# Optimization experiments

Hardware: AMD Instinct MI355X
Metric: run time of the kernel (lower is better)

Reference implementation:

```python
import jax, jax.numpy as jnp
import numpy as np

B, S, H, NH = 8, 1024, 1024, 16
D = H // NH          # attention_hidden_size = 64
V = S                # v_size must equal seq_len (mask broadcast)


def setup_inputs() -> dict:
    key = jax.random.key(0)
    ks = jax.random.split(key, 9)
    s = 0.02
    return {
        "q": jax.random.normal(ks[0], (B, S, H), jnp.float32),
        "k": jax.random.normal(ks[1], (B, S, H), jnp.float32),
        "v": jax.random.normal(ks[2], (B, S, H), jnp.float32),
        # per-head Q/K projections, stacked over heads: (NH, H, D)
        "Wq": jax.random.normal(ks[3], (NH, H, D), jnp.float32) * s,
        "bq": jax.random.normal(ks[4], (NH, D), jnp.float32) * s,
        "Wk": jax.random.normal(ks[5], (NH, H, D), jnp.float32) * s,
        "bk": jax.random.normal(ks[6], (NH, D), jnp.float32) * s,
        # shared V projection hidden -> v_size
        "Wv": jax.random.normal(ks[7], (H, V), jnp.float32) * s,
        "bv": jax.random.normal(ks[8], (V,), jnp.float32) * s,
    }


def reference(q, k, v, Wq, bq, Wk, bk, Wv, bv):
    d = Wq.shape[-1]
    scale = d ** (-0.5)
    # per-head projections, heads vectorized into leading axis n
    qh = jnp.einsum('bsh,nhd->nbsd', q, Wq) + bq[:, None, None, :]
    kh = jnp.einsum('bth,nhd->nbtd', k, Wk) + bk[:, None, None, :]
    vv = jnp.einsum('bth,hv->btv', v, Wv) + bv          # shared V: (B,S,V)
    seq = q.shape[1]
    mask = jnp.triu(jnp.full((seq, seq), -jnp.inf, dtype=q.dtype), 1)
    scores = jnp.einsum('nbsd,nbtd->nbst', qh, kh) * scale + mask
    p = jax.nn.softmax(scores, axis=-1)                  # (NH,B,S,S)
    # matmul against shared V then mean over heads (== stack + mean)
    out = jnp.einsum('nbst,btv->nbsv', p, vv).mean(axis=0)
    return out
```

## Files before the change

kernel.cpp:

```cpp
#include <hip/hip_runtime.h>


#define NHEAD 16
#define BATCH 8
#define SEQ   1024
#define HID   1024
#define DHEAD 64

typedef _Float16 f16;
typedef _Float16 f16x4 __attribute__((ext_vector_type(4)));
typedef _Float16 f16x8 __attribute__((ext_vector_type(8)));
typedef float    f32x4 __attribute__((ext_vector_type(4)));

__device__ __forceinline__ f32x4 mfma16(f16x8 a, f16x8 b, f32x4 c) {
  return __builtin_amdgcn_mfma_f32_16x16x32_f16(a, b, c, 0, 0, 0);
}

__device__ __forceinline__ void gload16(const f16* g, f16* l) {
  __builtin_amdgcn_global_load_lds(
      (const __attribute__((address_space(1))) void*)g,
      (__attribute__((address_space(3))) void*)l, 16, 0, 0);
}

__device__ __forceinline__ void stage_swz(const f16* __restrict__ g, int ldg,
                                          f16* lds, int nch, int tid) {
  for (int idx = tid; idx < nch; idx += 256) {
    int row = idx >> 3, c16 = idx & 7;
    int sc = c16 ^ (row & 7);
    gload16(g + (size_t)row * ldg + sc * 8, lds + (size_t)(idx & ~63) * 8);
  }
}

__device__ __forceinline__ f16x8 lds_frag(const f16* lds, int row, int c16) {
  int sc = c16 ^ (row & 7);
  return *(const f16x8*)&lds[row * 64 + sc * 8];
}


__global__ __launch_bounds__(256) void conv3(
    const float* __restrict__ q, const float* __restrict__ k,
    const float* __restrict__ v, f16* __restrict__ dq, f16* __restrict__ dk,
    f16* __restrict__ dv) {
  const float* src = blockIdx.z == 0 ? q : blockIdx.z == 1 ? k : v;
  f16* dst = blockIdx.z == 0 ? dq : blockIdx.z == 1 ? dk : dv;
  int i = (blockIdx.x * 256 + threadIdx.x) * 4;
  float4 f = *(const float4*)(src + i);
  f16x4 o = { (f16)f.x, (f16)f.y, (f16)f.z, (f16)f.w };
  *(f16x4*)(dst + i) = o;
}

__global__ __launch_bounds__(256) void tconv2(
    const float* __restrict__ s0, const float* __restrict__ s1,
    f16* __restrict__ d0, f16* __restrict__ d1, int R, int C, int half) {
  int z = blockIdx.z;
  const float* src; f16* dst;
  if (z < half) { src = s0 + (size_t)z * R * C; dst = d0 + (size_t)z * R * C; }
  else { src = s1 + (size_t)(z - half) * R * C; dst = d1 + (size_t)(z - half) * R * C; }
  const int c0 = blockIdx.x * 64, r0 = blockIdx.y * 64;
  __shared__ f16 t[64][72];
  const int tid = threadIdx.x;
#pragma unroll
  for (int i = 0; i < 4; i++) {
    int chunk = tid + i * 256;
    int row = chunk >> 4, c4 = chunk & 15;
    float4 f = *(const float4*)&src[(size_t)(r0 + row) * C + c0 + c4 * 4];
    f16x4 h = { (f16)f.x, (f16)f.y, (f16)f.z, (f16)f.w };
    *(f16x4*)&t[row][c4 * 4] = h;
  }
  __syncthreads();
  const int cc = tid >> 2, q = tid & 3;
  f16 tmp[16];
#pragma unroll
  for (int j = 0; j < 16; j++) tmp[j] = t[q * 16 + j][cc];
  *(f16x8*)&dst[(size_t)(c0 + cc) * R + r0 + q * 16] = *(f16x8*)&tmp[0];
  *(f16x8*)&dst[(size_t)(c0 + cc) * R + r0 + q * 16 + 8] = *(f16x8*)&tmp[8];
}


__device__ __forceinline__ void gemm_core(
    const f16* __restrict__ A, const f16* __restrict__ Bt, int K, int Kend,
    int row0, int col0, f16* la, f16* lb, int tid, f32x4 (&acc)[4][4]) {
  const int lane = tid & 63;
  const int wr = (tid >> 6) >> 1, wc = (tid >> 6) & 1;
  for (int k0 = 0; k0 < Kend; k0 += 64) {
    __syncthreads();
    stage_swz(A + (size_t)row0 * K + k0, K, la, 1024, tid);
    stage_swz(Bt + (size_t)col0 * K + k0, K, lb, 1024, tid);
    __syncthreads();
#pragma unroll
    for (int ks = 0; ks < 2; ks++) {
      f16x8 af[4], bfr[4];
#pragma unroll
      for (int mi = 0; mi < 4; mi++)
        af[mi] = lds_frag(la, wr * 64 + mi * 16 + (lane & 15), ks * 4 + (lane >> 4));
#pragma unroll
      for (int ni = 0; ni < 4; ni++)
        bfr[ni] = lds_frag(lb, wc * 64 + ni * 16 + (lane & 15), ks * 4 + (lane >> 4));
#pragma unroll
      for (int mi = 0; mi < 4; mi++)
#pragma unroll
        for (int ni = 0; ni < 4; ni++)
          acc[mi][ni] = mfma16(af[mi], bfr[ni], acc[mi][ni]);
    }
  }
}


__global__ __launch_bounds__(256) void proj_gemm(
    const f16* __restrict__ A0, const f16* __restrict__ A1,
    const f16* __restrict__ Bt0, const f16* __restrict__ Bt1,
    const float* __restrict__ bias0, const float* __restrict__ bias1,
    f16* __restrict__ C0, f16* __restrict__ C1) {
  const int which = blockIdx.z;
  const f16* A = which ? A1 : A0;
  const f16* Bt = which ? Bt1 : Bt0;
  const float* bias = which ? bias1 : bias0;
  f16* C = which ? C1 : C0;
  __shared__ alignas(16) f16 la[128 * 64];
  __shared__ alignas(16) f16 lb[128 * 64];
  const int tid = threadIdx.x, lane = tid & 63;
  const int wr = (tid >> 6) >> 1, wc = (tid >> 6) & 1;
  const int row0 = blockIdx.x * 128, col0 = blockIdx.y * 128;
  f32x4 acc[4][4];
#pragma unroll
  for (int i = 0; i < 4; i++)
#pragma unroll
    for (int j = 0; j < 4; j++) acc[i][j] = (f32x4){0.f, 0.f, 0.f, 0.f};
  gemm_core(A, Bt, HID, HID, row0, col0, la, lb, tid, acc);
#pragma unroll
  for (int mi = 0; mi < 4; mi++)
#pragma unroll
    for (int ni = 0; ni < 4; ni++)
#pragma unroll
      for (int r = 0; r < 4; r++) {
        int m = row0 + wr * 64 + mi * 16 + ((lane >> 4) << 2) + r;
        int j = col0 + wc * 64 + ni * 16 + (lane & 15);
        float val = acc[mi][ni][r] + bias[j];
        int bb = m >> 10, s = m & 1023, hn = j >> 6, d = j & 63;
        C[(((size_t)hn * BATCH + bb) * SEQ + s) * DHEAD + d] = (f16)val;
      }
}


__global__ __launch_bounds__(256) void vv_gemm(
    const f16* __restrict__ A, const f16* __restrict__ Bt,
    const float* __restrict__ bias, f16* __restrict__ C) {
  __shared__ alignas(16) f16 la[128 * 64];
  __shared__ alignas(16) f16 lb[128 * 64];
  const int tid = threadIdx.x, lane = tid & 63;
  const int wr = (tid >> 6) >> 1, wc = (tid >> 6) & 1;
  const int row0 = blockIdx.x * 128, col0 = blockIdx.y * 128;
  f32x4 acc[4][4];
#pragma unroll
  for (int i = 0; i < 4; i++)
#pragma unroll
    for (int j = 0; j < 4; j++) acc[i][j] = (f32x4){0.f, 0.f, 0.f, 0.f};
  gemm_core(A, Bt, HID, HID, row0, col0, la, lb, tid, acc);
#pragma unroll
  for (int mi = 0; mi < 4; mi++)
#pragma unroll
    for (int ni = 0; ni < 4; ni++)
#pragma unroll
      for (int r = 0; r < 4; r++) {
        int m = row0 + wr * 64 + mi * 16 + ((lane >> 4) << 2) + r;
        int j = col0 + wc * 64 + ni * 16 + (lane & 15);
        float val = acc[mi][ni][r] + bias[m];
        int bb = j >> 10, t = j & 1023;
        C[((size_t)bb * SEQ + m) * SEQ + t] = (f16)val;
      }
}


__global__ __launch_bounds__(256) void attn_stats(
    const f16* __restrict__ QH, const f16* __restrict__ KH,
    float* __restrict__ madj_ws) {
  const int flat = blockIdx.x;
  const int sb = 15 - (flat >> 7);
  const int nb = flat & 127;
  const int n = nb >> 3, b = nb & 7;
  const int s0 = sb * 64;
  const f16* qh = QH + ((size_t)n * BATCH + b) * SEQ * DHEAD;
  const f16* kh = KH + ((size_t)n * BATCH + b) * SEQ * DHEAD;

  const int tid = threadIdx.x, lane = tid & 63, wave = tid >> 6;
  const int lr = lane & 15;
  const int qg = lane >> 4;
  const int ch = qg << 3;

  f16x8 aq[4][2];
#pragma unroll
  for (int fi = 0; fi < 4; fi++) {
    const f16* qp = qh + (size_t)(s0 + fi * 16 + lr) * 64 + ch;
    aq[fi][0] = *(const f16x8*)qp;
    aq[fi][1] = *(const f16x8*)(qp + 32);
  }

  const float sl2e = 0.125f * 1.44269504088896f;
  float l_p[16];
#pragma unroll
  for (int i = 0; i < 16; i++) l_p[i] = 0.f;

  const int nt = (sb + 1) * 4;
  const int dstart = sb * 4;
  const int njw = (nt - wave + 3) >> 2;
  const f16* kp = kh + (size_t)lr * 64 + ch;

  f16x8 kA0, kA1, kB0, kB1;

#define LDK(jj, X0, X1) { const f16* p_ = kp + (size_t)(jj) * 1024; \
    X0 = *(const f16x8*)p_; X1 = *(const f16x8*)(p_ + 32); }

#define COMP(jj, X0, X1) { \
    f32x4 c_[4]; \
    _Pragma("unroll") for (int fi = 0; fi < 4; fi++) { \
      f32x4 cc = (f32x4){0.f, 0.f, 0.f, 0.f}; \
      cc = mfma16(aq[fi][0], X0, cc); cc = mfma16(aq[fi][1], X1, cc); \
      c_[fi] = cc; } \
    if ((jj) < dstart) { \
      _Pragma("unroll") for (int fi = 0; fi < 4; fi++) \
        _Pragma("unroll") for (int r = 0; r < 4; r++) \
          l_p[fi * 4 + r] += exp2f(c_[fi][r] * sl2e); \
    } else { \
      int tg_ = (jj) * 16 + lr; \
      _Pragma("unroll") for (int fi = 0; fi < 4; fi++) \
        _Pragma("unroll") for (int r = 0; r < 4; r++) { \
          int sg_ = s0 + fi * 16 + qg * 4 + r; \
          l_p[fi * 4 + r] += (tg_ <= sg_) ? exp2f(c_[fi][r] * sl2e) : 0.f; } } }

  LDK(wave, kA0, kA1);
  int idx = 0;
  for (; idx + 2 <= njw; idx += 2) {
    LDK(wave + (idx + 1) * 4, kB0, kB1);
    COMP(wave + idx * 4, kA0, kA1);
    if (idx + 2 < njw) LDK(wave + (idx + 2) * 4, kA0, kA1);
    COMP(wave + (idx + 1) * 4, kB0, kB1);
  }
  if (idx < njw) COMP(wave + idx * 4, kA0, kA1);
#undef LDK
#undef COMP

  __shared__ float lds_l[4][64];
#pragma unroll
  for (int i = 0; i < 16; i++) {
    float l = l_p[i];
    l += __shfl_xor(l, 1); l += __shfl_xor(l, 2);
    l += __shfl_xor(l, 4); l += __shfl_xor(l, 8);
    if (lr == 0) lds_l[wave][(i >> 2) * 16 + qg * 4 + (i & 3)] = l;
  }
  __syncthreads();
  if (tid < 64) {
    float l = lds_l[0][tid] + lds_l[1][tid] + lds_l[2][tid] + lds_l[3][tid];
    madj_ws[((size_t)n * BATCH + b) * SEQ + s0 + tid] = -__log2f(l) - 4.0f;
  }
}


__global__ __launch_bounds__(256) void attn_pbar(
    const f16* __restrict__ QH, const f16* __restrict__ KH,
    const float* __restrict__ madj_ws, f16* __restrict__ pp) {
  const int flat = blockIdx.x;
  const int wg = (flat & 7) * 144 + (flat >> 3);
  int f = wg % 72, sb = 0, tcid = 0;
  const int y = wg / 72;
  for (int s = 15; s >= 0; --s) {
    int c = (s >> 1) + 1;
    if (f < c) { sb = s; tcid = f; break; }
    f -= c;
  }
  const int s0 = sb * 64, t0 = tcid * 128;
  const int b = y >> 1, gg = y & 1;
  const int n0 = gg * 8;

  const int tid = threadIdx.x, lane = tid & 63, wave = tid >> 6;
  const float sl2e = 0.125f * 1.44269504088896f;
  const int lr = lane & 15, qg = lane >> 4, ch = qg << 3;

  int ntc = ((s0 + 63 - t0) >> 4) + 1;
  ntc = ntc > 8 ? 8 : ntc;
  const int j0 = wave, j1 = wave + 4;
  const bool has1 = j1 < ntc;

  const size_t HS = (size_t)BATCH * SEQ * DHEAD;
  const size_t MHS = (size_t)BATCH * SEQ;
  const f16* qbase = QH + (size_t)b * SEQ * DHEAD;
  const f16* kbase = KH + (size_t)b * SEQ * DHEAD;
  const float* mabase = madj_ws + (size_t)b * SEQ;

  float paccA[16], paccB[16];
#pragma unroll
  for (int i = 0; i < 16; i++) { paccA[i] = 0.f; paccB[i] = 0.f; }

  for (int nn = 0; nn < 8; nn++) {
    const int n = n0 + nn;
    const f16* qh = qbase + (size_t)n * HS;
    const f16* kh = kbase + (size_t)n * HS;

    f16x8 kA0, kA1, kB0, kB1;
    {
      const f16* p = kh + (size_t)(t0 + j0 * 16 + lr) * 64 + ch;
      kA0 = *(const f16x8*)p; kA1 = *(const f16x8*)(p + 32);
    }
    if (has1) {
      const f16* p = kh + (size_t)(t0 + j1 * 16 + lr) * 64 + ch;
      kB0 = *(const f16x8*)p; kB1 = *(const f16x8*)(p + 32);
    }
    f16x8 aq[4][2];
#pragma unroll
    for (int fi = 0; fi < 4; fi++) {
      const f16* qp = qh + (size_t)(s0 + fi * 16 + lr) * 64 + ch;
      aq[fi][0] = *(const f16x8*)qp;
      aq[fi][1] = *(const f16x8*)(qp + 32);
    }
    float ma[4][4];
#pragma unroll
    for (int fi = 0; fi < 4; fi++) {
      float4 m4 = *(const float4*)&mabase[(size_t)n * MHS + s0 + fi * 16 + qg * 4];
      ma[fi][0] = m4.x; ma[fi][1] = m4.y; ma[fi][2] = m4.z; ma[fi][3] = m4.w;
    }

#define PCOMP(jj, X0, X1, PC) { \
    int tg_ = t0 + (jj) * 16 + lr; \
    _Pragma("unroll") for (int fi = 0; fi < 4; fi++) { \
      f32x4 cc = (f32x4){0.f, 0.f, 0.f, 0.f}; \
      cc = mfma16(aq[fi][0], X0, cc); cc = mfma16(aq[fi][1], X1, cc); \
      _Pragma("unroll") for (int r = 0; r < 4; r++) { \
        int sg_ = s0 + fi * 16 + qg * 4 + r; \
        float p_ = exp2f(fmaf(cc[r], sl2e, ma[fi][r])); \
        PC[fi * 4 + r] += (tg_ <= sg_) ? p_ : 0.f; } } }

    PCOMP(j0, kA0, kA1, paccA);
    if (has1) PCOMP(j1, kB0, kB1, paccB);
#undef PCOMP
  }

  f16* out = pp + ((size_t)gg * BATCH + b) * SEQ * SEQ;
#pragma unroll
  for (int fi = 0; fi < 4; fi++) {
#pragma unroll
    for (int r = 0; r < 4; r++) {
      size_t row = (size_t)(s0 + fi * 16 + qg * 4 + r) * SEQ;
      out[row + t0 + j0 * 16 + lr] = (f16)paccA[fi * 4 + r];
      out[row + t0 + j1 * 16 + lr] = (f16)paccB[fi * 4 + r];
    }
  }
}


__global__ __launch_bounds__(256) void pv_gemm(
    const f16* __restrict__ pp, const f16* __restrict__ vvT,
    float* __restrict__ out) {
  const int b = blockIdx.z;
  const size_t GS = (size_t)BATCH * SEQ * SEQ;
  const f16* A0 = pp + (size_t)b * SEQ * SEQ;
  const f16* A1 = pp + GS + (size_t)b * SEQ * SEQ;
  const f16* Bt = vvT + (size_t)b * SEQ * SEQ;
  __shared__ alignas(16) f16 la0[128 * 64];
  __shared__ alignas(16) f16 la1[128 * 64];
  __shared__ alignas(16) f16 lb[128 * 64];
  const int tid = threadIdx.x, lane = tid & 63;
  const int wr = (tid >> 6) >> 1, wc = (tid >> 6) & 1;
  const int row0 = blockIdx.x * 128, col0 = blockIdx.y * 128;
  const int Kend = (row0 + 128 < SEQ) ? row0 + 128 : SEQ;

  f32x4 acc[4][4];
#pragma unroll
  for (int i = 0; i < 4; i++)
#pragma unroll
    for (int j = 0; j < 4; j++) acc[i][j] = (f32x4){0.f, 0.f, 0.f, 0.f};

  for (int k0 = 0; k0 < Kend; k0 += 64) {
    __syncthreads();
    stage_swz(A0 + (size_t)row0 * SEQ + k0, SEQ, la0, 1024, tid);
    stage_swz(A1 + (size_t)row0 * SEQ + k0, SEQ, la1, 1024, tid);
    stage_swz(Bt + (size_t)col0 * SEQ + k0, SEQ, lb, 1024, tid);
    __syncthreads();
#pragma unroll
    for (int ks = 0; ks < 2; ks++) {
      f16x8 a0[4], a1[4], bfr[4];
#pragma unroll
      for (int mi = 0; mi < 4; mi++) {
        a0[mi] = lds_frag(la0, wr * 64 + mi * 16 + (lane & 15), ks * 4 + (lane >> 4));
        a1[mi] = lds_frag(la1, wr * 64 + mi * 16 + (lane & 15), ks * 4 + (lane >> 4));
      }
#pragma unroll
      for (int ni = 0; ni < 4; ni++)
        bfr[ni] = lds_frag(lb, wc * 64 + ni * 16 + (lane & 15), ks * 4 + (lane >> 4));
#pragma unroll
      for (int mi = 0; mi < 4; mi++)
#pragma unroll
        for (int ni = 0; ni < 4; ni++) {
          acc[mi][ni] = mfma16(a0[mi], bfr[ni], acc[mi][ni]);
          acc[mi][ni] = mfma16(a1[mi], bfr[ni], acc[mi][ni]);
        }
    }
  }

#pragma unroll
  for (int mi = 0; mi < 4; mi++)
#pragma unroll
    for (int ni = 0; ni < 4; ni++)
#pragma unroll
      for (int r = 0; r < 4; r++) {
        int m = row0 + wr * 64 + mi * 16 + ((lane >> 4) << 2) + r;
        int j = col0 + wc * 64 + ni * 16 + (lane & 15);
        out[(size_t)b * SEQ * SEQ + (size_t)m * SEQ + j] = acc[mi][ni][r];
      }
}


extern "C" void kernel_launch(void* const* d_in, const int* in_sizes, int n_in,
                              void* d_out, int out_size, void* d_ws, size_t ws_size,
                              hipStream_t stream) {
  (void)in_sizes; (void)n_in; (void)out_size; (void)ws_size;
  const float* q  = (const float*)d_in[0];
  const float* k  = (const float*)d_in[1];
  const float* v  = (const float*)d_in[2];
  const float* Wq = (const float*)d_in[3];
  const float* bq = (const float*)d_in[4];
  const float* Wk = (const float*)d_in[5];
  const float* bk = (const float*)d_in[6];
  const float* Wv = (const float*)d_in[7];
  const float* bv = (const float*)d_in[8];
  float* out = (float*)d_out;

  const size_t EL  = (size_t)BATCH * SEQ * HID;
  const size_t WEL = (size_t)NHEAD * HID * DHEAD;

  char* ws = (char*)d_ws;
  f16* qbf = (f16*)ws;  ws += EL * 2;
  f16* kbf = (f16*)ws;  ws += EL * 2;
  f16* vbf = (f16*)ws;  ws += EL * 2;
  f16* WqT = (f16*)ws;  ws += WEL * 2;
  f16* WkT = (f16*)ws;  ws += WEL * 2;
  f16* WvT = (f16*)ws;  ws += WEL * 2;
  f16* QHb = (f16*)ws;  ws += EL * 2;
  f16* KHb = (f16*)ws;  ws += EL * 2;
  f16* vvT = (f16*)ws;  ws += EL * 2;
  float* madj_ws = (float*)ws; ws += (size_t)NHEAD * BATCH * SEQ * 4;
  f16* pp = qbf;

  conv3<<<dim3(8192, 1, 3), 256, 0, stream>>>(q, k, v, qbf, kbf, vbf);
  tconv2<<<dim3(1, 16, 32), 256, 0, stream>>>(Wq, Wk, WqT, WkT, 1024, 64, 16);
  tconv2<<<dim3(16, 16, 1), 256, 0, stream>>>(Wv, Wv, WvT, WvT, 1024, 1024, 1);

  proj_gemm<<<dim3(64, 8, 2), 256, 0, stream>>>(qbf, kbf, WqT, WkT, bq, bk,
                                                QHb, KHb);
  vv_gemm<<<dim3(8, 64, 1), 256, 0, stream>>>(WvT, vbf, bv, vvT);

  attn_stats<<<dim3(2048, 1, 1), 256, 0, stream>>>(QHb, KHb, madj_ws);
  attn_pbar<<<dim3(1152, 1, 1), 256, 0, stream>>>(QHb, KHb, madj_ws, pp);
  pv_gemm<<<dim3(8, 8, 8), 256, 0, stream>>>(pp, vvT, out);
}
```

Baseline: 240.7 us.

## Halve attn_pbar row tile, double-buffer per-head loads, skip mask on interior tiles

attn_pbar now covers 32 query rows per workgroup instead of 64, which doubles the grid to 2304 blocks and halves the per-thread accumulators. Launch bounds ask for 4 waves per SIMD. Q, K and row-max loads for the next head are software-pipelined into a second register set so they overlap the MFMA and exp work of the current head. The causal-mask compare is skipped on tiles that lie fully below the diagonal. The cost is more redundant K loads across the extra blocks and higher register pressure from the double buffers.

```diff
diff --git a/kernel.cpp b/kernel.cpp
--- a/kernel.cpp
+++ b/kernel.cpp
@@ -255,19 +255,20 @@
 }
 
 
-__global__ __launch_bounds__(256) void attn_pbar(
+__global__ __launch_bounds__(256, 4) void attn_pbar(
     const f16* __restrict__ QH, const f16* __restrict__ KH,
     const float* __restrict__ madj_ws, f16* __restrict__ pp) {
   const int flat = blockIdx.x;
-  const int wg = (flat & 7) * 144 + (flat >> 3);
-  int f = wg % 72, sb = 0, tcid = 0;
-  const int y = wg / 72;
-  for (int s = 15; s >= 0; --s) {
-    int c = (s >> 1) + 1;
+  const int wg = (flat & 7) * 288 + (flat >> 3);
+  int f = wg % 144;
+  const int y = wg / 144;
+  int sb = 0, tcid = 0;
+  for (int s = 31; s >= 0; --s) {
+    int c = (s >> 2) + 1;
     if (f < c) { sb = s; tcid = f; break; }
     f -= c;
   }
-  const int s0 = sb * 64, t0 = tcid * 128;
+  const int s0 = sb * 32, t0 = tcid * 128;
   const int b = y >> 1, gg = y & 1;
   const int n0 = gg * 8;
 
@@ -275,67 +276,77 @@
   const float sl2e = 0.125f * 1.44269504088896f;
   const int lr = lane & 15, qg = lane >> 4, ch = qg << 3;
 
-  int ntc = ((s0 + 63 - t0) >> 4) + 1;
+  int ntc = ((s0 + 31 - t0) >> 4) + 1;
   ntc = ntc > 8 ? 8 : ntc;
   const int j0 = wave, j1 = wave + 4;
-  const bool has1 = j1 < ntc;
+  const bool c0 = j0 < ntc, c1 = j1 < ntc;
 
   const size_t HS = (size_t)BATCH * SEQ * DHEAD;
   const size_t MHS = (size_t)BATCH * SEQ;
-  const f16* qbase = QH + (size_t)b * SEQ * DHEAD;
-  const f16* kbase = KH + (size_t)b * SEQ * DHEAD;
-  const float* mabase = madj_ws + (size_t)b * SEQ;
-
-  float paccA[16], paccB[16];
-#pragma unroll
-  for (int i = 0; i < 16; i++) { paccA[i] = 0.f; paccB[i] = 0.f; }
-
-  for (int nn = 0; nn < 8; nn++) {
-    const int n = n0 + nn;
-    const f16* qh = qbase + (size_t)n * HS;
-    const f16* kh = kbase + (size_t)n * HS;
-
-    f16x8 kA0, kA1, kB0, kB1;
-    {
-      const f16* p = kh + (size_t)(t0 + j0 * 16 + lr) * 64 + ch;
-      kA0 = *(const f16x8*)p; kA1 = *(const f16x8*)(p + 32);
-    }
-    if (has1) {
-      const f16* p = kh + (size_t)(t0 + j1 * 16 + lr) * 64 + ch;
-      kB0 = *(const f16x8*)p; kB1 = *(const f16x8*)(p + 32);
-    }
-    f16x8 aq[4][2];
-#pragma unroll
-    for (int fi = 0; fi < 4; fi++) {
-      const f16* qp = qh + (size_t)(s0 + fi * 16 + lr) * 64 + ch;
-      aq[fi][0] = *(const f16x8*)qp;
-      aq[fi][1] = *(const f16x8*)(qp + 32);
-    }
-    float ma[4][4];
-#pragma unroll
-    for (int fi = 0; fi < 4; fi++) {
-      float4 m4 = *(const float4*)&mabase[(size_t)n * MHS + s0 + fi * 16 + qg * 4];
-      ma[fi][0] = m4.x; ma[fi][1] = m4.y; ma[fi][2] = m4.z; ma[fi][3] = m4.w;
-    }
-
-#define PCOMP(jj, X0, X1, PC) { \
+  const f16* qptr = QH + ((size_t)n0 * BATCH + b) * SEQ * DHEAD +
+                    (size_t)(s0 + lr) * 64 + ch;
+  const f16* kptr = KH + ((size_t)n0 * BATCH + b) * SEQ * DHEAD +
+                    (size_t)(t0 + j0 * 16 + lr) * 64 + ch;
+  const float* mptr = madj_ws + ((size_t)n0 * BATCH + b) * SEQ + s0 + qg * 4;
+
+  float paccA[8], paccB[8];
+#pragma unroll
+  for (int i = 0; i < 8; i++) { paccA[i] = 0.f; paccB[i] = 0.f; }
+
+  f16x8 Xq0a, Xq0b, Xq1a, Xq1b, Xk0a, Xk0b, Xk1a, Xk1b;
+  float4 Xm0, Xm1;
+  f16x8 Yq0a, Yq0b, Yq1a, Yq1b, Yk0a, Yk0b, Yk1a, Yk1b;
+  float4 Ym0, Ym1;
+
+#define LOADH(h, q0a, q0b, q1a, q1b, k0a, k0b, k1a, k1b, m0, m1) { \
+    const f16* qp_ = qptr + (size_t)(h) * HS; \
+    q0a = *(const f16x8*)qp_;          q0b = *(const f16x8*)(qp_ + 32); \
+    q1a = *(const f16x8*)(qp_ + 1024); q1b = *(const f16x8*)(qp_ + 1024 + 32); \
+    const f16* kp_ = kptr + (size_t)(h) * HS; \
+    k0a = *(const f16x8*)kp_;          k0b = *(const f16x8*)(kp_ + 32); \
+    k1a = *(const f16x8*)(kp_ + 4096); k1b = *(const f16x8*)(kp_ + 4096 + 32); \
+    const float* mp_ = mptr + (size_t)(h) * MHS; \
+    m0 = *(const float4*)mp_; m1 = *(const float4*)(mp_ + 16); }
+
+#define TILE(jj, ka, kb, qa, qb, mm, pc, fi) { \
+    f32x4 cc = (f32x4){0.f, 0.f, 0.f, 0.f}; \
+    cc = mfma16(qa, ka, cc); \
+    cc = mfma16(qb, kb, cc); \
     int tg_ = t0 + (jj) * 16 + lr; \
-    _Pragma("unroll") for (int fi = 0; fi < 4; fi++) { \
-      f32x4 cc = (f32x4){0.f, 0.f, 0.f, 0.f}; \
-      cc = mfma16(aq[fi][0], X0, cc); cc = mfma16(aq[fi][1], X1, cc); \
-      _Pragma("unroll") for (int r = 0; r < 4; r++) { \
-        int sg_ = s0 + fi * 16 + qg * 4 + r; \
-        float p_ = exp2f(fmaf(cc[r], sl2e, ma[fi][r])); \
-        PC[fi * 4 + r] += (tg_ <= sg_) ? p_ : 0.f; } } }
-
-    PCOMP(j0, kA0, kA1, paccA);
-    if (has1) PCOMP(j1, kB0, kB1, paccB);
-#undef PCOMP
-  }
+    bool msk_ = (t0 + (jj) * 16 + 15) > (s0 + (fi) * 16); \
+    _Pragma("unroll") for (int r = 0; r < 4; r++) { \
+      float p_ = exp2f(fmaf(cc[r], sl2e, mm[r])); \
+      if (msk_) p_ = (tg_ <= s0 + (fi) * 16 + qg * 4 + r) ? p_ : 0.f; \
+      pc[(fi) * 4 + r] += p_; } }
+
+#define COMPH(q0a, q0b, q1a, q1b, k0a, k0b, k1a, k1b, m0, m1) { \
+    float mm0_[4] = {m0.x, m0.y, m0.z, m0.w}; \
+    float mm1_[4] = {m1.x, m1.y, m1.z, m1.w}; \
+    if (c0) { \
+      TILE(j0, k0a, k0b, q0a, q0b, mm0_, paccA, 0); \
+      TILE(j0, k0a, k0b, q1a, q1b, mm1_, paccA, 1); \
+    } \
+    if (c1) { \
+      TILE(j1, k1a, k1b, q0a, q0b, mm0_, paccB, 0); \
+      TILE(j1, k1a, k1b, q1a, q1b, mm1_, paccB, 1); \
+    } }
+
+  LOADH(0, Xq0a, Xq0b, Xq1a, Xq1b, Xk0a, Xk0b, Xk1a, Xk1b, Xm0, Xm1);
+#pragma unroll
+  for (int h = 0; h < 8; h += 2) {
+    LOADH(h + 1, Yq0a, Yq0b, Yq1a, Yq1b, Yk0a, Yk0b, Yk1a, Yk1b, Ym0, Ym1);
+    COMPH(Xq0a, Xq0b, Xq1a, Xq1b, Xk0a, Xk0b, Xk1a, Xk1b, Xm0, Xm1);
+    if (h + 2 < 8)
+      LOADH(h + 2, Xq0a, Xq0b, Xq1a, Xq1b, Xk0a, Xk0b, Xk1a, Xk1b, Xm0, Xm1);
+    COMPH(Yq0a, Yq0b, Yq1a, Yq1b, Yk0a, Yk0b, Yk1a, Yk1b, Ym0, Ym1);
+  }
+#undef LOADH
+#undef TILE
+#undef COMPH
 
   f16* out = pp + ((size_t)gg * BATCH + b) * SEQ * SEQ;
 #pragma unroll
-  for (int fi = 0; fi < 4; fi++) {
+  for (int fi = 0; fi < 2; fi++) {
 #pragma unroll
     for (int r = 0; r < 4; r++) {
       size_t row = (size_t)(s0 + fi * 16 + qg * 4 + r) * SEQ;
@@ -448,6 +459,6 @@
   vv_gemm<<<dim3(8, 64, 1), 256, 0, stream>>>(WvT, vbf, bv, vvT);
 
   attn_stats<<<dim3(2048, 1, 1), 256, 0, stream>>>(QHb, KHb, madj_ws);
-  attn_pbar<<<dim3(1152, 1, 1), 256, 0, stream>>>(QHb, KHb, madj_ws, pp);
+  attn_pbar<<<dim3(2304, 1, 1), 256, 0, stream>>>(QHb, KHb, madj_ws, pp);
   pv_gemm<<<dim3(8, 8, 8), 256, 0, stream>>>(pp, vvT, out);
 }
```

Result: slower. 247.0 us (+2.6%).

## Rewrite P-bar kernel as LDS-staged 128x128 tiled GEMM over lower triangle

Applied to the files above, without the earlier changes.

Replaces the per-wave register-fragment attn_pbar kernel (64x128 tiles, direct global loads of Q/K per head) with a 128x128 tiled kernel that stages Q and K head tiles into swizzled LDS and computes a 4x4 MFMA block per wave. Only lower-triangular tile pairs are launched, and the causal mask is applied only on diagonal tiles. This is meant to raise data reuse and MFMA density and cut redundant global loads. In exchange it uses fewer, larger blocks (576 vs 1152), adds two syncthreads per head, and does more masked work inside the diagonal tiles.

```diff
diff --git a/kernel.cpp b/kernel.cpp
--- a/kernel.cpp
+++ b/kernel.cpp
@@ -255,94 +255,103 @@
 }
 
 
-__global__ __launch_bounds__(256) void attn_pbar(
+__global__ __launch_bounds__(256) void pbar_gemm(
     const f16* __restrict__ QH, const f16* __restrict__ KH,
     const float* __restrict__ madj_ws, f16* __restrict__ pp) {
-  const int flat = blockIdx.x;
-  const int wg = (flat & 7) * 144 + (flat >> 3);
-  int f = wg % 72, sb = 0, tcid = 0;
-  const int y = wg / 72;
-  for (int s = 15; s >= 0; --s) {
-    int c = (s >> 1) + 1;
-    if (f < c) { sb = s; tcid = f; break; }
-    f -= c;
-  }
-  const int s0 = sb * 64, t0 = tcid * 128;
-  const int b = y >> 1, gg = y & 1;
-  const int n0 = gg * 8;
-
-  const int tid = threadIdx.x, lane = tid & 63, wave = tid >> 6;
+  int ti = blockIdx.x, rb = 0, cb = 0;
+  {
+    int t = ti;
+#pragma unroll
+    for (int r = 0; r < 8; ++r) {
+      if (t <= r) { rb = r; cb = t; break; }
+      t -= r + 1;
+    }
+  }
+  const int r0 = rb * 128, c0 = cb * 128;
+  const int y = blockIdx.y;
+  const int b = y >> 1, g = y & 1;
+  const int n0 = g * 8;
+  const bool diag = (rb == cb);
+
+  __shared__ alignas(16) f16 la[128 * 64];
+  __shared__ alignas(16) f16 lb[128 * 64];
+
+  const int tid = threadIdx.x, lane = tid & 63;
+  const int wr = (tid >> 6) >> 1, wc = (tid >> 6) & 1;
+  const int lr = lane & 15, qg = lane >> 4;
   const float sl2e = 0.125f * 1.44269504088896f;
-  const int lr = lane & 15, qg = lane >> 4, ch = qg << 3;
-
-  int ntc = ((s0 + 63 - t0) >> 4) + 1;
-  ntc = ntc > 8 ? 8 : ntc;
-  const int j0 = wave, j1 = wave + 4;
-  const bool has1 = j1 < ntc;
-
-  const size_t HS = (size_t)BATCH * SEQ * DHEAD;
-  const size_t MHS = (size_t)BATCH * SEQ;
-  const f16* qbase = QH + (size_t)b * SEQ * DHEAD;
-  const f16* kbase = KH + (size_t)b * SEQ * DHEAD;
-  const float* mabase = madj_ws + (size_t)b * SEQ;
-
-  float paccA[16], paccB[16];
-#pragma unroll
-  for (int i = 0; i < 16; i++) { paccA[i] = 0.f; paccB[i] = 0.f; }
-
-  for (int nn = 0; nn < 8; nn++) {
-    const int n = n0 + nn;
-    const f16* qh = qbase + (size_t)n * HS;
-    const f16* kh = kbase + (size_t)n * HS;
-
-    f16x8 kA0, kA1, kB0, kB1;
-    {
-      const f16* p = kh + (size_t)(t0 + j0 * 16 + lr) * 64 + ch;
-      kA0 = *(const f16x8*)p; kA1 = *(const f16x8*)(p + 32);
+
+  f32x4 pacc[4][4];
+#pragma unroll
+  for (int i = 0; i < 4; i++)
+#pragma unroll
+    for (int j = 0; j < 4; j++) pacc[i][j] = (f32x4){0.f, 0.f, 0.f, 0.f};
+
+  for (int h = 0; h < 8; ++h) {
+    const int n = n0 + h;
+    const f16* qh = QH + ((size_t)n * BATCH + b) * SEQ * DHEAD;
+    const f16* kh = KH + ((size_t)n * BATCH + b) * SEQ * DHEAD;
+
+    __syncthreads();
+    stage_swz(qh + (size_t)r0 * 64, 64, la, 1024, tid);
+    stage_swz(kh + (size_t)c0 * 64, 64, lb, 1024, tid);
+    __syncthreads();
+
+    f32x4 acc[4][4];
+#pragma unroll
+    for (int i = 0; i < 4; i++)
+#pragma unroll
+      for (int j = 0; j < 4; j++) acc[i][j] = (f32x4){0.f, 0.f, 0.f, 0.f};
+
+#pragma unroll
+    for (int ks = 0; ks < 2; ks++) {
+      f16x8 af[4], bfr[4];
+#pragma unroll
+      for (int mi = 0; mi < 4; mi++)
+        af[mi] = lds_frag(la, wr * 64 + mi * 16 + lr, ks * 4 + qg);
+#pragma unroll
+      for (int ni = 0; ni < 4; ni++)
+        bfr[ni] = lds_frag(lb, wc * 64 + ni * 16 + lr, ks * 4 + qg);
+#pragma unroll
+      for (int mi = 0; mi < 4; mi++)
+#pragma unroll
+        for (int ni = 0; ni < 4; ni++)
+          acc[mi][ni] = mfma16(af[mi], bfr[ni], acc[mi][ni]);
     }
-    if (has1) {
-      const f16* p = kh + (size_t)(t0 + j1 * 16 + lr) * 64 + ch;
-      kB0 = *(const f16x8*)p; kB1 = *(const f16x8*)(p + 32);
+
+    const float* mb = madj_ws + ((size_t)n * BATCH + b) * SEQ + r0 +
+                      wr * 64 + qg * 4;
+#pragma unroll
+    for (int mi = 0; mi < 4; mi++) {
+      float4 m4 = *(const float4*)(mb + mi * 16);
+      float ma[4] = {m4.x, m4.y, m4.z, m4.w};
+#pragma unroll
+      for (int ni = 0; ni < 4; ni++) {
+        int tg = c0 + wc * 64 + ni * 16 + lr;
+#pragma unroll
+        for (int r = 0; r < 4; r++) {
+          float p = exp2f(fmaf(acc[mi][ni][r], sl2e, ma[r]));
+          if (diag) {
+            int sg = r0 + wr * 64 + mi * 16 + qg * 4 + r;
+            p = (tg <= sg) ? p : 0.f;
+          }
+          pacc[mi][ni][r] += p;
+        }
+      }
     }
-    f16x8 aq[4][2];
-#pragma unroll
-    for (int fi = 0; fi < 4; fi++) {
-      const f16* qp = qh + (size_t)(s0 + fi * 16 + lr) * 64 + ch;
-      aq[fi][0] = *(const f16x8*)qp;
-      aq[fi][1] = *(const f16x8*)(qp + 32);
-    }
-    float ma[4][4];
-#pragma unroll
-    for (int fi = 0; fi < 4; fi++) {
-      float4 m4 = *(const float4*)&mabase[(size_t)n * MHS + s0 + fi * 16 + qg * 4];
-      ma[fi][0] = m4.x; ma[fi][1] = m4.y; ma[fi][2] = m4.z; ma[fi][3] = m4.w;
-    }
-
-#define PCOMP(jj, X0, X1, PC) { \
-    int tg_ = t0 + (jj) * 16 + lr; \
-    _Pragma("unroll") for (int fi = 0; fi < 4; fi++) { \
-      f32x4 cc = (f32x4){0.f, 0.f, 0.f, 0.f}; \
-      cc = mfma16(aq[fi][0], X0, cc); cc = mfma16(aq[fi][1], X1, cc); \
-      _Pragma("unroll") for (int r = 0; r < 4; r++) { \
-        int sg_ = s0 + fi * 16 + qg * 4 + r; \
-        float p_ = exp2f(fmaf(cc[r], sl2e, ma[fi][r])); \
-        PC[fi * 4 + r] += (tg_ <= sg_) ? p_ : 0.f; } } }
-
-    PCOMP(j0, kA0, kA1, paccA);
-    if (has1) PCOMP(j1, kB0, kB1, paccB);
-#undef PCOMP
-  }
-
-  f16* out = pp + ((size_t)gg * BATCH + b) * SEQ * SEQ;
-#pragma unroll
-  for (int fi = 0; fi < 4; fi++) {
-#pragma unroll
-    for (int r = 0; r < 4; r++) {
-      size_t row = (size_t)(s0 + fi * 16 + qg * 4 + r) * SEQ;
-      out[row + t0 + j0 * 16 + lr] = (f16)paccA[fi * 4 + r];
-      out[row + t0 + j1 * 16 + lr] = (f16)paccB[fi * 4 + r];
-    }
-  }
+  }
+
+  f16* out = pp + ((size_t)g * BATCH + b) * SEQ * SEQ;
+#pragma unroll
+  for (int mi = 0; mi < 4; mi++)
+#pragma unroll
+    for (int ni = 0; ni < 4; ni++)
+#pragma unroll
+      for (int r = 0; r < 4; r++) {
+        int m = r0 + wr * 64 + mi * 16 + qg * 4 + r;
+        int j = c0 + wc * 64 + ni * 16 + lr;
+        out[(size_t)m * SEQ + j] = (f16)pacc[mi][ni][r];
+      }
 }
 
 
@@ -448,6 +457,6 @@
   vv_gemm<<<dim3(8, 64, 1), 256, 0, stream>>>(WvT, vbf, bv, vvT);
 
   attn_stats<<<dim3(2048, 1, 1), 256, 0, stream>>>(QHb, KHb, madj_ws);
-  attn_pbar<<<dim3(1152, 1, 1), 256, 0, stream>>>(QHb, KHb, madj_ws, pp);
+  pbar_gemm<<<dim3(36, 16, 1), 256, 0, stream>>>(QHb, KHb, madj_ws, pp);
   pv_gemm<<<dim3(8, 8, 8), 256, 0, stream>>>(pp, vvT, out);
 }
```

New measurement: 238.3 us. No clear change (-1.0%).
